# Optimization experiments

Measured on AMD Instinct MI355X. Metric: run time of the kernel, lower is better.

The kernel has to match this reference:

```python
import jax, jax.numpy as jnp
import numpy as np

NUM_HEADS = 16
NUM_KV_HEADS = 4
ROPE_BASE = 10000.0
TRAIN_SEQ_LEN = 2048


def _rms_norm(x):
    eps = jnp.asarray(jnp.finfo(x.dtype).eps, x.dtype)
    return x * jax.lax.rsqrt(jnp.mean(x * x, axis=-1, keepdims=True) + eps)


def _rope_cos_sin(seq_len, head_dim, dtype):
    # seq_len <= TRAIN_SEQ_LEN -> no NTK rescaling, matches Rotary buffer path
    half = head_dim // 2
    inv_freq = 1.0 / (ROPE_BASE ** (jnp.arange(0, head_dim, 2, dtype=jnp.float32) / head_dim))
    t = jnp.arange(seq_len, dtype=jnp.float32)
    freqs = jnp.outer(t, inv_freq)  # [S, half]
    cos = jnp.cos(freqs)[None, :, None, :].astype(dtype)
    sin = jnp.sin(freqs)[None, :, None, :].astype(dtype)
    return cos, sin


def _apply_rotary(x, cos, sin):
    half = x.shape[-1] // 2
    x1, x2 = x[..., :half], x[..., half:]
    return jnp.concatenate([x1 * cos + x2 * sin, -x1 * sin + x2 * cos], axis=-1)


def setup_inputs() -> dict:
    key = jax.random.key(0)
    ks = jax.random.split(key, 5)
    B, S, D = 2, 2048, 2048
    kv_dim = NUM_KV_HEADS * (D // NUM_HEADS)
    sw = 0.02
    return {
        "x": jax.random.normal(ks[0], (B, S, D), jnp.float32),
        "Wq": jax.random.normal(ks[1], (D, D), jnp.float32) * sw,
        "Wk": jax.random.normal(ks[2], (kv_dim, D), jnp.float32) * sw,
        "Wv": jax.random.normal(ks[3], (kv_dim, D), jnp.float32) * sw,
        "Wproj": jax.random.normal(ks[4], (D, D), jnp.float32) * sw,
        "q_gain": jnp.ones((NUM_HEADS,), jnp.float32),
    }


def reference(x, Wq, Wk, Wv, Wproj, q_gain):
    B, S, D = x.shape
    H, Hkv = NUM_HEADS, NUM_KV_HEADS
    hd = D // H
    r = H // Hkv

    q = (x @ Wq.T).reshape(B, S, H, hd)
    k = (x @ Wk.T).reshape(B, S, Hkv, hd)
    v = (x @ Wv.T).reshape(B, S, Hkv, hd)

    q = _rms_norm(q)
    k = _rms_norm(k)

    cos, sin = _rope_cos_sin(S, hd, q.dtype)
    q = _apply_rotary(q, cos, sin)
    k = _apply_rotary(k, cos, sin)
    q = q * q_gain.astype(q.dtype)[None, None, :, None]

    # GQA: repeat kv heads (repeat_interleave along head dim)
    k = jnp.repeat(k, r, axis=2)  # [B,S,H,hd]
    v = jnp.repeat(v, r, axis=2)

    scale = 1.0 / jnp.sqrt(jnp.asarray(hd, q.dtype))
    scores = jnp.einsum("bqhd,bkhd->bhqk", q, k) * scale
    causal = jnp.tril(jnp.ones((S, S), dtype=bool))
    scores = jnp.where(causal[None, None], scores, jnp.asarray(-jnp.inf, scores.dtype))
    attn = jax.nn.softmax(scores, axis=-1)
    y = jnp.einsum("bhqk,bkhd->bqhd", attn, v)

    return y.reshape(B, S, D) @ Wproj.T
```

## Files before the change

kernel.cpp:

```cpp
#include <hip/hip_runtime.h>

#define D_MODEL 2048
#define SEQ 2048
#define BATCH 2
#define NH 16
#define NKV 4
#define HD 128
#define KVD (NKV * HD)
#define QKVN (D_MODEL + 2 * KVD)
#define MROWS (BATCH * SEQ)

typedef __attribute__((ext_vector_type(8))) short short8;
typedef __attribute__((ext_vector_type(4))) float f32x4;

__device__ __forceinline__ unsigned short f2bf(float f) {
    union { float f; unsigned int u; } v; v.f = f;
    unsigned int r = (v.u + 0x7FFFu + ((v.u >> 16) & 1u)) >> 16;
    return (unsigned short)r;
}

__device__ __forceinline__ unsigned short f2bf_pos(float f) {
    union { float f; unsigned int u; } v; v.f = f;
    return (unsigned short)((v.u + 0x8000u) >> 16);
}

__device__ __forceinline__ float bf2f(unsigned short u) {
    union { float f; unsigned int i; } v; v.i = ((unsigned int)u) << 16;
    return v.f;
}

__device__ __forceinline__ void async16(const void* g, void* l) {
    __builtin_amdgcn_global_load_lds((const __attribute__((address_space(1))) void*)g,
                                     (__attribute__((address_space(3))) void*)l, 16, 0, 0);
}

__global__ __launch_bounds__(256) void cast_all(const float* __restrict__ x,
                                                const float* __restrict__ wq,
                                                const float* __restrict__ wk,
                                                const float* __restrict__ wv,
                                                const float* __restrict__ wp,
                                                unsigned short* __restrict__ xb,
                                                unsigned short* __restrict__ wqkv,
                                                unsigned short* __restrict__ wpb) {
    int i = blockIdx.x * 256 + threadIdx.x;
    const float4* s; ushort4* d; int j;
    if (i < 2097152)      { s = (const float4*)x;  d = (ushort4*)xb;             j = i; }
    else if (i < 3145728) { s = (const float4*)wq; d = (ushort4*)wqkv;           j = i - 2097152; }
    else if (i < 3407872) { s = (const float4*)wk; d = (ushort4*)wqkv + 1048576; j = i - 3145728; }
    else if (i < 3670016) { s = (const float4*)wv; d = (ushort4*)wqkv + 1310720; j = i - 3407872; }
    else                  { s = (const float4*)wp; d = (ushort4*)wpb;            j = i - 3670016; }
    float4 v = s[j];
    ushort4 o;
    o.x = f2bf(v.x); o.y = f2bf(v.y); o.z = f2bf(v.z); o.w = f2bf(v.w);
    d[j] = o;
}

__global__ __launch_bounds__(256) void gemm_qkv(const unsigned short* __restrict__ A,
                                                const unsigned short* __restrict__ W,
                                                const float* __restrict__ gain,
                                                unsigned short* __restrict__ qbuf,
                                                unsigned short* __restrict__ kbuf,
                                                unsigned short* __restrict__ vtb) {
    __shared__ unsigned short smem[128 * 137];
    unsigned short* Al = smem;
    unsigned short* Bl = smem + 8192;
    unsigned short* tile = smem;
    const int K = D_MODEL;
    const int tid  = threadIdx.x;
    const int lane = tid & 63;
    const int wave = tid >> 6;
    const int qm   = lane & 15;
    const int quad = lane >> 4;
    const int m0 = blockIdx.y * 128;
    const int bx = blockIdx.x;
    const int n0 = bx * 128;
    const int wm = (wave >> 1) * 64;
    const int wn = (wave & 1) * 64;

    f32x4 acc[4][4];
#pragma unroll
    for (int i = 0; i < 4; i++)
#pragma unroll
        for (int j = 0; j < 4; j++) acc[i][j] = (f32x4){0.f, 0.f, 0.f, 0.f};

    const int r1 = tid >> 2;
    const int c1 = (((tid & 3) ^ ((tid >> 3) & 3)) * 8);
    const unsigned short* Ag = A + (size_t)(m0 + r1) * K + c1;
    const unsigned short* Wg = W + (size_t)(n0 + r1) * K + c1;
    const int stg = wave * 512;
    const int swq = ((qm >> 1) & 3) * 8;

#define STG_Q(khv) \
    async16(Ag + (khv) * 32,                  &Al[(khv) * 4096 + stg]); \
    async16(Ag + (khv) * 32 + (size_t)64 * K, &Al[(khv) * 4096 + 2048 + stg]); \
    async16(Wg + (khv) * 32,                  &Bl[(khv) * 4096 + stg]); \
    async16(Wg + (khv) * 32 + (size_t)64 * K, &Bl[(khv) * 4096 + 2048 + stg]);

#define CMP_Q(khv) { \
    short8 af[4], bfr[4]; \
    _Pragma("unroll") \
    for (int i = 0; i < 4; i++) { \
        af[i]  = *(const short8*)&Al[(khv) * 4096 + (wm + i * 16 + qm) * 32 + (quad * 8 ^ swq)]; \
        bfr[i] = *(const short8*)&Bl[(khv) * 4096 + (wn + i * 16 + qm) * 32 + (quad * 8 ^ swq)]; \
    } \
    _Pragma("unroll") \
    for (int mi = 0; mi < 4; mi++) \
        _Pragma("unroll") \
        for (int ni = 0; ni < 4; ni++) \
            acc[mi][ni] = __builtin_amdgcn_mfma_f32_16x16x32_bf16(af[mi], bfr[ni], acc[mi][ni], 0, 0, 0); \
}

    for (int kt = 0; kt < K; kt += 64) {
        STG_Q(0)
        STG_Q(1)
        Ag += 64; Wg += 64;
        __syncthreads();
        CMP_Q(0)
        CMP_Q(1)
        __syncthreads();
    }
#undef STG_Q
#undef CMP_Q

#pragma unroll
    for (int mi = 0; mi < 4; mi++)
#pragma unroll
        for (int r = 0; r < 4; r++) {
            int row = wm + mi * 16 + quad * 4 + r;
#pragma unroll
            for (int ni = 0; ni < 4; ni++)
                tile[row * 137 + wn + ni * 16 + qm] = f2bf(acc[mi][ni][r]);
        }
    __syncthreads();

    const int s_base = m0 & 2047;
    const int bb = m0 >> 11;
    if (bx < 20) {
        const bool isq = bx < 16;
        const float g = isq ? gain[bx] * 0.12751744f : 1.0f;
        unsigned short* dst = isq
            ? qbuf + ((size_t)(bb * NH + bx) * SEQ + s_base) * HD
            : kbuf + ((size_t)(bb * NKV + (bx - 16)) * SEQ + s_base) * HD;
        const float invf = __builtin_amdgcn_exp2f(-(float)lane * 0.20761871f - 2.6514961f);
        for (int rr = 0; rr < 32; rr++) {
            int row = wave * 32 + rr;
            float x1 = bf2f(tile[row * 137 + lane]);
            float x2 = bf2f(tile[row * 137 + 64 + lane]);
            float ss = x1 * x1 + x2 * x2;
            ss += __shfl_xor(ss, 1);  ss += __shfl_xor(ss, 2);  ss += __shfl_xor(ss, 4);
            ss += __shfl_xor(ss, 8);  ss += __shfl_xor(ss, 16); ss += __shfl_xor(ss, 32);
            float rs = rsqrtf(ss * (1.0f / 128.0f) + 1.1920929e-07f);
            float rev = (float)(s_base + row) * invf;
            rev -= truncf(rev);
            float sn = __builtin_amdgcn_sinf(rev);
            float cs = __builtin_amdgcn_cosf(rev);
            float a1 = x1 * rs, a2 = x2 * rs;
            float o1 = (a1 * cs + a2 * sn) * g;
            float o2 = (a2 * cs - a1 * sn) * g;
            dst[(size_t)row * HD + lane]      = f2bf(o1);
            dst[(size_t)row * HD + 64 + lane] = f2bf(o2);
        }
    } else {
        const int hk = bx - 20;
        unsigned short* dst = vtb + ((size_t)(bb * NKV + hk) * HD) * SEQ + s_base;
        const int sc = (tid & 31) * 4;
        const int d0 = tid >> 5;
#pragma unroll
        for (int i = 0; i < 16; i++) {
            int d = d0 + 8 * i;
            ushort4 ov;
            ov.x = tile[(sc + 0) * 137 + d];
            ov.y = tile[(sc + 1) * 137 + d];
            ov.z = tile[(sc + 2) * 137 + d];
            ov.w = tile[(sc + 3) * 137 + d];
            *(ushort4*)(dst + (size_t)d * SEQ + sc) = ov;
        }
    }
}

__global__ __launch_bounds__(256) void gemm_bt(const unsigned short* __restrict__ A,
                                               const unsigned short* __restrict__ W,
                                               float* __restrict__ C, int M, int N, int K) {
    __shared__ unsigned short smem[32768];
    unsigned short* Al = smem;
    unsigned short* Bl = smem + 16384;
    const int tid  = threadIdx.x;
    const int lane = tid & 63;
    const int wave = tid >> 6;
    const int qm   = lane & 15;
    const int quad = lane >> 4;
    const int m0 = blockIdx.y * 128;
    const int n0 = blockIdx.x * 128;
    const int wm = (wave >> 1) * 64;
    const int wn = (wave & 1) * 64;

    f32x4 acc[4][4];
#pragma unroll
    for (int i = 0; i < 4; i++)
#pragma unroll
        for (int j = 0; j < 4; j++) acc[i][j] = (f32x4){0.f, 0.f, 0.f, 0.f};

    const int r1 = tid >> 2;
    const int c1 = (((tid & 3) ^ ((tid >> 3) & 3)) * 8);
    const unsigned short* Ag = A + (size_t)(m0 + r1) * K + c1;
    const unsigned short* Wg = W + (size_t)(n0 + r1) * K + c1;
    const int stg = wave * 512;
    const int swq = ((qm >> 1) & 3) * 8;

#define STG_B(khv, bufv) \
    async16(Ag + (khv) * 32,                  &Al[(bufv) * 8192 + (khv) * 4096 + stg]); \
    async16(Ag + (khv) * 32 + (size_t)64 * K, &Al[(bufv) * 8192 + (khv) * 4096 + 2048 + stg]); \
    async16(Wg + (khv) * 32,                  &Bl[(bufv) * 8192 + (khv) * 4096 + stg]); \
    async16(Wg + (khv) * 32 + (size_t)64 * K, &Bl[(bufv) * 8192 + (khv) * 4096 + 2048 + stg]);

#define CMP_B(bufv, khv) { \
    short8 af[4], bfr[4]; \
    _Pragma("unroll") \
    for (int i = 0; i < 4; i++) { \
        af[i]  = *(const short8*)&Al[(bufv) * 8192 + (khv) * 4096 + (wm + i * 16 + qm) * 32 + (quad * 8 ^ swq)]; \
        bfr[i] = *(const short8*)&Bl[(bufv) * 8192 + (khv) * 4096 + (wn + i * 16 + qm) * 32 + (quad * 8 ^ swq)]; \
    } \
    __builtin_amdgcn_s_setprio(1); \
    _Pragma("unroll") \
    for (int mi = 0; mi < 4; mi++) \
        _Pragma("unroll") \
        for (int ni = 0; ni < 4; ni++) \
            acc[mi][ni] = __builtin_amdgcn_mfma_f32_16x16x32_bf16(af[mi], bfr[ni], acc[mi][ni], 0, 0, 0); \
    __builtin_amdgcn_s_setprio(0); \
}

    STG_B(0, 0)
    STG_B(1, 0)
    Ag += 64; Wg += 64;
    asm volatile("s_waitcnt vmcnt(4)\n\ts_barrier" ::: "memory");

    int buf = 0;
    for (int t = 0; t < K / 64 - 1; ++t) {
        STG_B(0, buf ^ 1)
        CMP_B(buf, 0)
        asm volatile("s_waitcnt vmcnt(4)\n\ts_barrier" ::: "memory");
        STG_B(1, buf ^ 1)
        CMP_B(buf, 1)
        asm volatile("s_waitcnt vmcnt(4)\n\ts_barrier" ::: "memory");
        Ag += 64; Wg += 64;
        buf ^= 1;
    }
    CMP_B(buf, 0)
    asm volatile("s_waitcnt vmcnt(0)\n\ts_barrier" ::: "memory");
    CMP_B(buf, 1)
#undef STG_B
#undef CMP_B

#pragma unroll
    for (int mi = 0; mi < 4; mi++) {
#pragma unroll
        for (int r = 0; r < 4; r++) {
            int row = m0 + wm + mi * 16 + quad * 4 + r;
            float* Crow = C + (size_t)row * N + n0 + wn + qm;
#pragma unroll
            for (int ni = 0; ni < 4; ni++) Crow[ni * 16] = acc[mi][ni][r];
        }
    }
}

__global__ __launch_bounds__(256, 4) void attn(const unsigned short* __restrict__ qb,
                                               const unsigned short* __restrict__ kb,
                                               const unsigned short* __restrict__ vt,
                                               const float* __restrict__ gain,
                                               unsigned short* __restrict__ y) {
    __shared__ unsigned short Ks[8192];
    __shared__ unsigned short Vs[8192];
    __shared__ unsigned short plds[4][1024];
    const int tid  = threadIdx.x;
    const int lane = tid & 63;
    const int wave = tid >> 6;
    const int bh   = blockIdx.x & 31;
    const int g4   = blockIdx.x >> 5;
    const int gg = g4 & 7;
    const int gs = g4 >> 3;
    const int qt64 = (gs == 0) ? gg : (gs == 1) ? (31 - gg) : (gs == 2) ? (8 + gg) : (23 - gg);
    const int h = bh & 15;
    const int b = bh >> 4;
    const int qm   = lane & 15;
    const int quad = lane >> 4;
    const int q0    = qt64 * 64;
    const int qrow0 = q0 + wave * 16;
    const float M = 17.0f * fabsf(gain[h]);

    const unsigned short* Qp = qb + (((size_t)(b * NH + h)) * SEQ + qrow0) * HD;
    const unsigned short* Kp = kb + ((size_t)(b * NKV + (h >> 2))) * SEQ * HD;
    const unsigned short* Vp = vt + ((size_t)(b * NKV + (h >> 2))) * HD * SEQ;

    short8 qf[4];
#pragma unroll
    for (int c = 0; c < 4; c++)
        qf[c] = *(const short8*)(Qp + qm * HD + c * 32 + quad * 8);

    f32x4 o[8];
#pragma unroll
    for (int t = 0; t < 8; t++) o[t] = (f32x4){0.f, 0.f, 0.f, 0.f};
    float lr[4] = {0.f, 0.f, 0.f, 0.f};

    const unsigned short* KsA = Kp + (size_t)(tid >> 4) * HD + (((tid & 15) ^ (tid >> 4)) & 15) * 8;
    const unsigned short* VsA = Vp + (size_t)(tid >> 3) * SEQ + (((tid & 7) ^ ((tid >> 3) & 7)) * 8);
    char* KsB = (char*)Ks + wave * 1024;
    char* VsB = (char*)Vs + wave * 1024;
    unsigned short* P = &plds[wave][0];

    const int kvend = q0 + 64;
    for (int kv0 = 0; kv0 < kvend; kv0 += 64) {
#pragma unroll
        for (int i = 0; i < 4; i++) {
            async16(KsA + (size_t)(16 * i) * HD,  KsB + i * 4096);
            async16(VsA + (size_t)(32 * i) * SEQ, VsB + i * 4096);
        }
        KsA += (size_t)64 * HD;
        VsA += 64;
        __syncthreads();

        f32x4 s[4];
#pragma unroll
        for (int g = 0; g < 4; g++) s[g] = (f32x4){0.f, 0.f, 0.f, 0.f};
#pragma unroll
        for (int c = 0; c < 4; c++) {
#pragma unroll
            for (int g = 0; g < 4; g++) {
                short8 kf = *(const short8*)&Ks[(g * 16 + qm) * 128 + (((c * 4 + quad) ^ qm) * 8)];
                s[g] = __builtin_amdgcn_mfma_f32_16x16x32_bf16(qf[c], kf, s[g], 0, 0, 0);
            }
        }
        if (kv0 + 63 > qrow0) {
#pragma unroll
            for (int g = 0; g < 4; g++)
#pragma unroll
                for (int r = 0; r < 4; r++) {
                    int qg = qrow0 + quad * 4 + r;
                    if (kv0 + g * 16 + qm > qg) s[g][r] = -3.0e38f;
                }
        }
        float p[4][4];
#pragma unroll
        for (int g = 0; g < 4; g++)
#pragma unroll
            for (int r = 0; r < 4; r++) {
                p[g][r] = __builtin_amdgcn_exp2f(s[g][r] - M);
                lr[r] += p[g][r];
            }
#pragma unroll
        for (int g = 0; g < 4; g++)
#pragma unroll
            for (int r = 0; r < 4; r++) {
                int rowp = quad * 4 + r;
                P[rowp * 64 + (((g * 2 + (qm >> 3)) ^ (rowp & 7)) * 8) + (qm & 7)] = f2bf_pos(p[g][r]);
            }
        short8 pa[2];
#pragma unroll
        for (int ka = 0; ka < 2; ka++)
            pa[ka] = *(const short8*)&P[qm * 64 + (((ka * 4 + quad) ^ (qm & 7)) * 8)];
#pragma unroll
        for (int t = 0; t < 8; t++) {
#pragma unroll
            for (int ka = 0; ka < 2; ka++) {
                short8 vf = *(const short8*)&Vs[(t * 16 + qm) * 64 + (((ka * 4 + quad) ^ (qm & 7)) * 8)];
                o[t] = __builtin_amdgcn_mfma_f32_16x16x32_bf16(pa[ka], vf, o[t], 0, 0, 0);
            }
        }
        __syncthreads();
    }
    float rl[4];
#pragma unroll
    for (int r = 0; r < 4; r++) {
        float l = lr[r];
        l += __shfl_xor(l, 1);
        l += __shfl_xor(l, 2);
        l += __shfl_xor(l, 4);
        l += __shfl_xor(l, 8);
        rl[r] = 1.0f / l;
    }
#pragma unroll
    for (int t = 0; t < 8; t++) {
#pragma unroll
        for (int r = 0; r < 4; r++) {
            size_t row = (size_t)(b * SEQ + qrow0 + quad * 4 + r);
            y[row * D_MODEL + h * HD + t * 16 + qm] = f2bf(o[t][r] * rl[r]);
        }
    }
}

extern "C" void kernel_launch(void* const* d_in, const int* in_sizes, int n_in,
                              void* d_out, int out_size, void* d_ws, size_t ws_size,
                              hipStream_t stream) {
    const float* x  = (const float*)d_in[0];
    const float* Wq = (const float*)d_in[1];
    const float* Wk = (const float*)d_in[2];
    const float* Wv = (const float*)d_in[3];
    const float* Wp = (const float*)d_in[4];
    const float* qg = (const float*)d_in[5];

    char* ws = (char*)d_ws;
    unsigned short* xb   = (unsigned short*)(ws + 0);
    unsigned short* wqkv = (unsigned short*)(ws + 16777216);
    unsigned short* wp   = (unsigned short*)(ws + 29360128);
    unsigned short* qbuf = (unsigned short*)(ws + 37748736);
    unsigned short* kbuf = (unsigned short*)(ws + 54525952);
    unsigned short* vtb  = (unsigned short*)(ws + 58720256);
    unsigned short* y    = xb;

    cast_all<<<18432, 256, 0, stream>>>(x, Wq, Wk, Wv, Wp, xb, wqkv, wp);
    gemm_qkv<<<dim3(24, 32), 256, 0, stream>>>(xb, wqkv, qg, qbuf, kbuf, vtb);
    attn<<<1024, 256, 0, stream>>>(qbuf, kbuf, vtb, qg, y);
    gemm_bt<<<dim3(16, 32), 256, 0, stream>>>(y, wp, (float*)d_out, MROWS, D_MODEL, D_MODEL);
}
```

Measured before the change: 292.7 us.

## Pipeline QKV GEMM loads with K32 double buffering and shrink output GEMM LDS

The QKV projection GEMM now issues the next 32-wide K slice of async global-to-LDS loads while computing the current one, using a two-slot ping-pong with vmcnt waits and barriers. Previously it loaded a whole 64-wide step and then computed behind full __syncthreads, so loads and math did not overlap. The output projection GEMM moves from a 64-wide double buffer (64 KB LDS) to the same 32-wide ping-pong in 32 KB, which may allow more resident blocks per CU. The cost is twice as many barriers per K step and a hard-coded trip count of 31 that assumes K=2048, so gemm_bt is no longer correct for other K values.

```diff
diff --git a/kernel.cpp b/kernel.cpp
--- a/kernel.cpp
+++ b/kernel.cpp
@@ -62,8 +62,6 @@
                                                 unsigned short* __restrict__ kbuf,
                                                 unsigned short* __restrict__ vtb) {
     __shared__ unsigned short smem[128 * 137];
-    unsigned short* Al = smem;
-    unsigned short* Bl = smem + 8192;
     unsigned short* tile = smem;
     const int K = D_MODEL;
     const int tid  = threadIdx.x;
@@ -90,35 +88,46 @@
     const int stg = wave * 512;
     const int swq = ((qm >> 1) & 3) * 8;
 
-#define STG_Q(khv) \
-    async16(Ag + (khv) * 32,                  &Al[(khv) * 4096 + stg]); \
-    async16(Ag + (khv) * 32 + (size_t)64 * K, &Al[(khv) * 4096 + 2048 + stg]); \
-    async16(Wg + (khv) * 32,                  &Bl[(khv) * 4096 + stg]); \
-    async16(Wg + (khv) * 32 + (size_t)64 * K, &Bl[(khv) * 4096 + 2048 + stg]);
-
-#define CMP_Q(khv) { \
+#define STG_Q(bufv) \
+    async16(Ag,                  &smem[(bufv) * 4096 + stg]); \
+    async16(Ag + (size_t)64 * K, &smem[(bufv) * 4096 + 2048 + stg]); \
+    async16(Wg,                  &smem[8192 + (bufv) * 4096 + stg]); \
+    async16(Wg + (size_t)64 * K, &smem[8192 + (bufv) * 4096 + 2048 + stg]); \
+    Ag += 32; Wg += 32;
+
+#define CMP_Q(bufv) { \
     short8 af[4], bfr[4]; \
     _Pragma("unroll") \
     for (int i = 0; i < 4; i++) { \
-        af[i]  = *(const short8*)&Al[(khv) * 4096 + (wm + i * 16 + qm) * 32 + (quad * 8 ^ swq)]; \
-        bfr[i] = *(const short8*)&Bl[(khv) * 4096 + (wn + i * 16 + qm) * 32 + (quad * 8 ^ swq)]; \
+        af[i]  = *(const short8*)&smem[(bufv) * 4096 + (wm + i * 16 + qm) * 32 + (quad * 8 ^ swq)]; \
+        bfr[i] = *(const short8*)&smem[8192 + (bufv) * 4096 + (wn + i * 16 + qm) * 32 + (quad * 8 ^ swq)]; \
     } \
+    __builtin_amdgcn_s_setprio(1); \
     _Pragma("unroll") \
     for (int mi = 0; mi < 4; mi++) \
         _Pragma("unroll") \
         for (int ni = 0; ni < 4; ni++) \
             acc[mi][ni] = __builtin_amdgcn_mfma_f32_16x16x32_bf16(af[mi], bfr[ni], acc[mi][ni], 0, 0, 0); \
-}
-
-    for (int kt = 0; kt < K; kt += 64) {
+    __builtin_amdgcn_s_setprio(0); \
+}
+
+    STG_Q(0)
+    for (int t = 0; t < 31; ++t) {
+        STG_Q(1)
+        asm volatile("s_waitcnt vmcnt(4)\n\ts_barrier" ::: "memory");
+        CMP_Q(0)
+        asm volatile("s_barrier" ::: "memory");
         STG_Q(0)
-        STG_Q(1)
-        Ag += 64; Wg += 64;
-        __syncthreads();
-        CMP_Q(0)
+        asm volatile("s_waitcnt vmcnt(4)\n\ts_barrier" ::: "memory");
         CMP_Q(1)
-        __syncthreads();
-    }
+        asm volatile("s_barrier" ::: "memory");
+    }
+    STG_Q(1)
+    asm volatile("s_waitcnt vmcnt(4)\n\ts_barrier" ::: "memory");
+    CMP_Q(0)
+    asm volatile("s_waitcnt vmcnt(0)\n\ts_barrier" ::: "memory");
+    CMP_Q(1)
+    __syncthreads();
 #undef STG_Q
 #undef CMP_Q
 
@@ -181,9 +190,7 @@
 __global__ __launch_bounds__(256) void gemm_bt(const unsigned short* __restrict__ A,
                                                const unsigned short* __restrict__ W,
                                                float* __restrict__ C, int M, int N, int K) {
-    __shared__ unsigned short smem[32768];
-    unsigned short* Al = smem;
-    unsigned short* Bl = smem + 16384;
+    __shared__ unsigned short smem[16384];
     const int tid  = threadIdx.x;
     const int lane = tid & 63;
     const int wave = tid >> 6;
@@ -207,18 +214,19 @@
     const int stg = wave * 512;
     const int swq = ((qm >> 1) & 3) * 8;
 
-#define STG_B(khv, bufv) \
-    async16(Ag + (khv) * 32,                  &Al[(bufv) * 8192 + (khv) * 4096 + stg]); \
-    async16(Ag + (khv) * 32 + (size_t)64 * K, &Al[(bufv) * 8192 + (khv) * 4096 + 2048 + stg]); \
-    async16(Wg + (khv) * 32,                  &Bl[(bufv) * 8192 + (khv) * 4096 + stg]); \
-    async16(Wg + (khv) * 32 + (size_t)64 * K, &Bl[(bufv) * 8192 + (khv) * 4096 + 2048 + stg]);
-
-#define CMP_B(bufv, khv) { \
+#define STG_B(bufv) \
+    async16(Ag,                  &smem[(bufv) * 4096 + stg]); \
+    async16(Ag + (size_t)64 * K, &smem[(bufv) * 4096 + 2048 + stg]); \
+    async16(Wg,                  &smem[8192 + (bufv) * 4096 + stg]); \
+    async16(Wg + (size_t)64 * K, &smem[8192 + (bufv) * 4096 + 2048 + stg]); \
+    Ag += 32; Wg += 32;
+
+#define CMP_B(bufv) { \
     short8 af[4], bfr[4]; \
     _Pragma("unroll") \
     for (int i = 0; i < 4; i++) { \
-        af[i]  = *(const short8*)&Al[(bufv) * 8192 + (khv) * 4096 + (wm + i * 16 + qm) * 32 + (quad * 8 ^ swq)]; \
-        bfr[i] = *(const short8*)&Bl[(bufv) * 8192 + (khv) * 4096 + (wn + i * 16 + qm) * 32 + (quad * 8 ^ swq)]; \
+        af[i]  = *(const short8*)&smem[(bufv) * 4096 + (wm + i * 16 + qm) * 32 + (quad * 8 ^ swq)]; \
+        bfr[i] = *(const short8*)&smem[8192 + (bufv) * 4096 + (wn + i * 16 + qm) * 32 + (quad * 8 ^ swq)]; \
     } \
     __builtin_amdgcn_s_setprio(1); \
     _Pragma("unroll") \
@@ -229,25 +237,22 @@
     __builtin_amdgcn_s_setprio(0); \
 }
 
-    STG_B(0, 0)
-    STG_B(1, 0)
-    Ag += 64; Wg += 64;
+    STG_B(0)
+    for (int t = 0; t < 31; ++t) {
+        STG_B(1)
+        asm volatile("s_waitcnt vmcnt(4)\n\ts_barrier" ::: "memory");
+        CMP_B(0)
+        asm volatile("s_barrier" ::: "memory");
+        STG_B(0)
+        asm volatile("s_waitcnt vmcnt(4)\n\ts_barrier" ::: "memory");
+        CMP_B(1)
+        asm volatile("s_barrier" ::: "memory");
+    }
+    STG_B(1)
     asm volatile("s_waitcnt vmcnt(4)\n\ts_barrier" ::: "memory");
-
-    int buf = 0;
-    for (int t = 0; t < K / 64 - 1; ++t) {
-        STG_B(0, buf ^ 1)
-        CMP_B(buf, 0)
-        asm volatile("s_waitcnt vmcnt(4)\n\ts_barrier" ::: "memory");
-        STG_B(1, buf ^ 1)
-        CMP_B(buf, 1)
-        asm volatile("s_waitcnt vmcnt(4)\n\ts_barrier" ::: "memory");
-        Ag += 64; Wg += 64;
-        buf ^= 1;
-    }
-    CMP_B(buf, 0)
+    CMP_B(0)
     asm volatile("s_waitcnt vmcnt(0)\n\ts_barrier" ::: "memory");
-    CMP_B(buf, 1)
+    CMP_B(1)
 #undef STG_B
 #undef CMP_B
 
```

Result: no change. 292.2 us (-0.2%).
